# Kernel optimization log

Hardware: AMD Instinct MI355X
Metric: run time of the kernel (lower is better)

## Reference

```python
import jax, jax.numpy as jnp
import numpy as np
from jax import lax


def _gaussian_kernel(sigma=2.0, size=5):
    # matches torch: arange(-size//2 + 1, size//2 + 1) == [-2,-1,0,1,2] for size=5
    r = np.arange(-(size // 2), size // 2 + 1, dtype=np.float32)
    xx, yy = np.meshgrid(r, r, indexing='ij')
    k = np.exp(-(xx ** 2 + yy ** 2) / (2.0 * sigma ** 2))
    return jnp.asarray(k / k.sum(), dtype=jnp.float32)


SCHARR_0 = jnp.array([[3, 0, -3], [10, 0, -10], [3, 0, -3]], dtype=jnp.float32)
SCHARR_90 = jnp.array([[3, 10, 3], [0, 0, 0], [-3, -10, -3]], dtype=jnp.float32)
LAPLACIAN = jnp.array([[0, -1, 0], [-1, 4, -1], [0, -1, 0]], dtype=jnp.float32)
GAUSS = _gaussian_kernel(2.0, 5)
SCHARR_W = 1.0
LAP_W = 0.1


def dwconv(x, k, pad):
    # depthwise conv: x [B,C,H,W], k [kh,kw] shared across channels
    C = x.shape[1]
    kern = jnp.broadcast_to(k[None, None], (C, 1) + k.shape)
    return lax.conv_general_dilated(
        x, kern, window_strides=(1, 1), padding=[(pad, pad), (pad, pad)],
        feature_group_count=C, dimension_numbers=('NCHW', 'OIHW', 'NCHW'))


def conv1x1(x, w, b):
    # x [B,C,H,W], w [O,C], b [O]
    return jnp.einsum('bchw,oc->bohw', x, w) + b[None, :, None, None]


def setup_inputs() -> dict:
    key = jax.random.key(0)
    ks = jax.random.split(key, 6)
    B, C, H, W = 4, 256, 256, 256
    s = 0.05
    return {
        'x': jax.random.normal(ks[0], (B, C, H, W), jnp.float32),
        'w_in': jax.random.normal(ks[1], (64, 256), jnp.float32) * s,
        'b_in': jnp.zeros((64,), jnp.float32),
        'w_fc1': jax.random.normal(ks[2], (4, 64), jnp.float32) * s,
        'b_fc1': jnp.zeros((4,), jnp.float32),
        'w_fc2': jax.random.normal(ks[3], (64, 4), jnp.float32) * s,
        'b_fc2': jnp.zeros((64,), jnp.float32),
        'w_out': jax.random.normal(ks[4], (64, 64), jnp.float32) * s,
        'b_out': jnp.zeros((64,), jnp.float32),
    }


def reference(x, w_in, b_in, w_fc1, b_fc1, w_fc2, b_fc2, w_out, b_out):
    x = conv1x1(x, w_in, b_in)                       # [B,64,H,W]
    sm = dwconv(x, GAUSS, pad=2)                     # gaussian blur
    g0 = dwconv(sm, SCHARR_0, pad=1)
    g90 = dwconv(sm, SCHARR_90, pad=1)
    scharr_mag = SCHARR_W * jnp.maximum(jnp.abs(g0), jnp.abs(g90))
    lap = LAP_W * jnp.abs(dwconv(sm, LAPLACIAN, pad=1))
    edge = scharr_mag + lap
    edge = jnp.clip(edge / (edge.max() + 1e-8), 0.0, 1.0)
    # channel attention (SE)
    pooled = edge.mean(axis=(2, 3), keepdims=True)   # [B,64,1,1]
    h = jax.nn.relu(conv1x1(pooled, w_fc1, b_fc1))
    scale = jax.nn.sigmoid(conv1x1(h, w_fc2, b_fc2))
    edge = edge * scale
    return conv1x1(edge, w_out, b_out)
```

## Files before the change

kernel.cpp:

```cpp
#include <hip/hip_runtime.h>
#include <math.h>


#define HW 65536

#define WS_WT    0ull
#define WS_Y     65536ull
#define WS_EDGE  (65536ull + 67108864ull)
#define WS_SMALL (65536ull + 134217728ull)

__global__ __launch_bounds__(256) void k0_prep(const float* __restrict__ w_in,
                                               float* __restrict__ wT,
                                               unsigned* __restrict__ small) {
    const int tid = threadIdx.x;
    for (int i = tid; i < 512; i += 256) small[i] = 0u;
    for (int i = tid; i < 64 * 256; i += 256) {
        int o = i >> 8, c = i & 255;
        wT[c * 64 + o] = w_in[i];
    }
}

#define K1_COMP(xv, wrp)                                                      \
    {                                                                         \
        float4 w0 = *(const float4*)(wrp);                                    \
        float4 w1 = *(const float4*)((wrp) + 4);                              \
        float4 w2 = *(const float4*)((wrp) + 8);                              \
        float4 w3 = *(const float4*)((wrp) + 12);                             \
        float wf[16] = {w0.x,w0.y,w0.z,w0.w, w1.x,w1.y,w1.z,w1.w,             \
                        w2.x,w2.y,w2.z,w2.w, w3.x,w3.y,w3.z,w3.w};            \
        _Pragma("unroll")                                                     \
        for (int oi = 0; oi < 16; ++oi) {                                     \
            acc[0][oi] = fmaf((xv).x, wf[oi], acc[0][oi]);                    \
            acc[1][oi] = fmaf((xv).y, wf[oi], acc[1][oi]);                    \
            acc[2][oi] = fmaf((xv).z, wf[oi], acc[2][oi]);                    \
            acc[3][oi] = fmaf((xv).w, wf[oi], acc[3][oi]);                    \
        }                                                                     \
    }

__global__ __launch_bounds__(256) void k1_convin(const float* __restrict__ x,
                                                 const float* __restrict__ wT,
                                                 const float* __restrict__ b_in,
                                                 float* __restrict__ y) {
    __shared__ float ws[64 * 64];
    const int tid  = threadIdx.x;
    const int lane = tid & 63;
    const int wv   = tid >> 6;
    const int blk  = blockIdx.x;
    const int b    = blk >> 8;
    const int pbase = ((blk & 255) << 8) + (wv << 6) + ((lane & 15) << 2);
    const int og    = (lane >> 4) << 4;

    const float* xp = x + (size_t)(b << 8) * HW + pbase;

    float acc[4][16];
#pragma unroll
    for (int oi = 0; oi < 16; ++oi) {
        float bv = b_in[og + oi];
        acc[0][oi] = bv; acc[1][oi] = bv; acc[2][oi] = bv; acc[3][oi] = bv;
    }

    float4 xb0 = *(const float4*)(xp + 0 * (size_t)HW);
    float4 xb1 = *(const float4*)(xp + 1 * (size_t)HW);
    float4 xb2 = *(const float4*)(xp + 2 * (size_t)HW);
    float4 xb3 = *(const float4*)(xp + 3 * (size_t)HW);

#pragma unroll 1
    for (int ch = 0; ch < 4; ++ch) {
        __syncthreads();
        const float4* src = (const float4*)(wT + (ch << 6) * 64);
        float4* dst = (float4*)ws;
        for (int i = tid; i < 1024; i += 256) dst[i] = src[i];
        __syncthreads();

#pragma unroll 1
        for (int cc = 0; cc < 64; cc += 4) {
            const int gn = ((ch << 6) + cc + 4) & 255;
            float4 n0 = *(const float4*)(xp + (size_t)(gn    ) * HW);
            float4 n1 = *(const float4*)(xp + (size_t)(gn + 1) * HW);
            float4 n2 = *(const float4*)(xp + (size_t)(gn + 2) * HW);
            float4 n3 = *(const float4*)(xp + (size_t)(gn + 3) * HW);

            const float* wr = ws + (cc << 6) + og;
            K1_COMP(xb0, wr);
            K1_COMP(xb1, wr + 64);
            K1_COMP(xb2, wr + 128);
            K1_COMP(xb3, wr + 192);

            xb0 = n0; xb1 = n1; xb2 = n2; xb3 = n3;
        }
    }

    float* yb = y + (size_t)(b << 6) * HW + pbase;
#pragma unroll
    for (int oi = 0; oi < 16; ++oi) {
        float4 o4 = {acc[0][oi], acc[1][oi], acc[2][oi], acc[3][oi]};
        *(float4*)(yb + (size_t)(og + oi) * HW) = o4;
    }
}

__global__ __launch_bounds__(256) void k2_edge(const float* __restrict__ y,
                                               float* __restrict__ edge,
                                               unsigned* __restrict__ umax,
                                               float* __restrict__ sums) {
    const int lane = threadIdx.x & 63;
    const int task = blockIdx.x * 4 + (threadIdx.x >> 6);
    const int plane = task >> 4;
    const int r0 = (task & 15) << 4;
    const float* yp = y + (size_t)plane * HW;
    float* ep = edge + (size_t)plane * HW;
    const int col4 = lane << 2;

    const float g = 0.60653066f, G = 0.88249690f;
    const float S1 = 2.f * g + 2.f * G + 1.f;
    const float inv2 = 1.f / (S1 * S1);

    float4 h0{}, h1{}, h2{}, h3{}, h4{};
    float4 s0{}, s1{}, s2{};
    float lmax = 0.f, lsum = 0.f;

    for (int j = r0 - 3; j <= r0 + 18; ++j) {
        float4 v = {0.f, 0.f, 0.f, 0.f};
        if (j >= 0 && j < 256) v = *(const float4*)(yp + j * 256 + col4);
        float lz = __shfl(v.z, lane - 1), lw = __shfl(v.w, lane - 1);
        float rx = __shfl(v.x, lane + 1), ry = __shfl(v.y, lane + 1);
        if (lane == 0)  { lz = 0.f; lw = 0.f; }
        if (lane == 63) { rx = 0.f; ry = 0.f; }
        float4 hv;
        hv.x = fmaf(g, lz,  fmaf(G, lw,  fmaf(G, v.y, fmaf(g, v.z, v.x))));
        hv.y = fmaf(g, lw,  fmaf(G, v.x, fmaf(G, v.z, fmaf(g, v.w, v.y))));
        hv.z = fmaf(g, v.x, fmaf(G, v.y, fmaf(G, v.w, fmaf(g, rx, v.z))));
        hv.w = fmaf(g, v.y, fmaf(G, v.z, fmaf(G, rx,  fmaf(g, ry, v.w))));
        h0 = h1; h1 = h2; h2 = h3; h3 = h4; h4 = hv;

        if (j >= r0 + 1) {
            float4 sv;
            sv.x = (g * (h0.x + h4.x) + G * (h1.x + h3.x) + h2.x) * inv2;
            sv.y = (g * (h0.y + h4.y) + G * (h1.y + h3.y) + h2.y) * inv2;
            sv.z = (g * (h0.z + h4.z) + G * (h1.z + h3.z) + h2.z) * inv2;
            sv.w = (g * (h0.w + h4.w) + G * (h1.w + h3.w) + h2.w) * inv2;
            s0 = s1; s1 = s2; s2 = sv;

            if (j >= r0 + 3) {
                const int er = j - 3;
                float4 A = s0, B = s1, C = s2;
                float Alw = __shfl(A.w, lane - 1), Arx = __shfl(A.x, lane + 1);
                float Blw = __shfl(B.w, lane - 1), Brx = __shfl(B.x, lane + 1);
                float Clw = __shfl(C.w, lane - 1), Crx = __shfl(C.x, lane + 1);
                if (lane == 0)  { Alw = 0.f; Blw = 0.f; Clw = 0.f; }
                if (lane == 63) { Arx = 0.f; Brx = 0.f; Crx = 0.f; }
                if (er == 0)   { A = float4{}; Alw = 0.f; Arx = 0.f; }
                if (er == 255) { C = float4{}; Clw = 0.f; Crx = 0.f; }
                float A6[6] = {Alw, A.x, A.y, A.z, A.w, Arx};
                float B6[6] = {Blw, B.x, B.y, B.z, B.w, Brx};
                float C6[6] = {Clw, C.x, C.y, C.z, C.w, Crx};
                float4 e4;
                float* ev = (float*)&e4;
#pragma unroll
                for (int k = 0; k < 4; ++k) {
                    float g0  = 3.f * (A6[k] - A6[k+2]) + 10.f * (B6[k] - B6[k+2])
                              + 3.f * (C6[k] - C6[k+2]);
                    float g90 = 3.f * (A6[k] - C6[k]) + 10.f * (A6[k+1] - C6[k+1])
                              + 3.f * (A6[k+2] - C6[k+2]);
                    float lap = 4.f * B6[k+1] - B6[k] - B6[k+2] - A6[k+1] - C6[k+1];
                    float e = fmaxf(fabsf(g0), fabsf(g90)) + 0.1f * fabsf(lap);
                    ev[k] = e;
                    lmax = fmaxf(lmax, e);
                    lsum += e;
                }
                *(float4*)(ep + er * 256 + col4) = e4;
            }
        }
    }

    for (int off = 32; off > 0; off >>= 1) {
        lmax = fmaxf(lmax, __shfl_down(lmax, off));
        lsum += __shfl_down(lsum, off);
    }
    if (lane == 0) {
        atomicMax(umax, __float_as_uint(lmax));
        atomicAdd(&sums[plane], lsum);
    }
}

__global__ __launch_bounds__(256) void k3_se(const unsigned* __restrict__ umax,
                                             const float* __restrict__ sums,
                                             const float* __restrict__ w_fc1,
                                             const float* __restrict__ b_fc1,
                                             const float* __restrict__ w_fc2,
                                             const float* __restrict__ b_fc2,
                                             const float* __restrict__ w_out,
                                             float* __restrict__ w_eff) {
    const int tid = threadIdx.x;
    const int b = tid >> 6, o = tid & 63;
    const float mx = __uint_as_float(*umax);
    const float inv = 1.f / (mx + 1e-8f);
    __shared__ float coef[256];

    float h[4];
#pragma unroll
    for (int j = 0; j < 4; ++j) h[j] = b_fc1[j];
    for (int c = 0; c < 64; ++c) {
        float pooled = sums[b * 64 + c] * inv * (1.f / 65536.f);
#pragma unroll
        for (int j = 0; j < 4; ++j) h[j] = fmaf(pooled, w_fc1[j * 64 + c], h[j]);
    }
#pragma unroll
    for (int j = 0; j < 4; ++j) h[j] = fmaxf(h[j], 0.f);
    float z = b_fc2[o];
#pragma unroll
    for (int j = 0; j < 4; ++j) z = fmaf(h[j], w_fc2[o * 4 + j], z);
    float sc = 1.f / (1.f + expf(-z));
    coef[tid] = sc * inv;
    __syncthreads();
    for (int c = 0; c < 64; ++c)
        w_eff[((b * 64) + c) * 64 + o] = w_out[o * 64 + c] * coef[b * 64 + c];
}

__global__ __launch_bounds__(256) void k4_out(const float* __restrict__ edge,
                                              const float* __restrict__ w_eff,
                                              const float* __restrict__ b_out,
                                              float* __restrict__ out) {
    __shared__ float ws[64 * 64];
    const int tid  = threadIdx.x;
    const int lane = tid & 63;
    const int wv   = tid >> 6;
    const int blk  = blockIdx.x;
    const int b    = blk >> 8;
    const int pbase = ((blk & 255) << 8) + (wv << 6) + ((lane & 15) << 2);
    const int og    = (lane >> 4) << 4;

    {
        const float4* src = (const float4*)(w_eff + b * 4096);
        float4* dst = (float4*)ws;
        for (int i = tid; i < 1024; i += 256) dst[i] = src[i];
    }

    const float* eb = edge + (size_t)(b << 6) * HW + pbase;
    float acc[4][16];
#pragma unroll
    for (int oi = 0; oi < 16; ++oi) {
        float bv = b_out[og + oi];
        acc[0][oi] = bv; acc[1][oi] = bv; acc[2][oi] = bv; acc[3][oi] = bv;
    }

    float4 xb0 = *(const float4*)(eb + 0 * (size_t)HW);
    float4 xb1 = *(const float4*)(eb + 1 * (size_t)HW);
    float4 xb2 = *(const float4*)(eb + 2 * (size_t)HW);
    float4 xb3 = *(const float4*)(eb + 3 * (size_t)HW);

    __syncthreads();

#pragma unroll 1
    for (int cc = 0; cc < 64; cc += 4) {
        const int gn = (cc + 4) & 63;
        float4 n0 = *(const float4*)(eb + (size_t)(gn    ) * HW);
        float4 n1 = *(const float4*)(eb + (size_t)(gn + 1) * HW);
        float4 n2 = *(const float4*)(eb + (size_t)(gn + 2) * HW);
        float4 n3 = *(const float4*)(eb + (size_t)(gn + 3) * HW);

        const float* wr = ws + (cc << 6) + og;
        K1_COMP(xb0, wr);
        K1_COMP(xb1, wr + 64);
        K1_COMP(xb2, wr + 128);
        K1_COMP(xb3, wr + 192);

        xb0 = n0; xb1 = n1; xb2 = n2; xb3 = n3;
    }

    float* ob = out + (size_t)(b << 6) * HW + pbase;
#pragma unroll
    for (int oi = 0; oi < 16; ++oi) {
        float4 o4 = {acc[0][oi], acc[1][oi], acc[2][oi], acc[3][oi]};
        *(float4*)(ob + (size_t)(og + oi) * HW) = o4;
    }
}

extern "C" void kernel_launch(void* const* d_in, const int* in_sizes, int n_in,
                              void* d_out, int out_size, void* d_ws, size_t ws_size,
                              hipStream_t stream) {
    const float* x     = (const float*)d_in[0];
    const float* w_in  = (const float*)d_in[1];
    const float* b_in  = (const float*)d_in[2];
    const float* w_fc1 = (const float*)d_in[3];
    const float* b_fc1 = (const float*)d_in[4];
    const float* w_fc2 = (const float*)d_in[5];
    const float* b_fc2 = (const float*)d_in[6];
    const float* w_out = (const float*)d_in[7];
    const float* b_out = (const float*)d_in[8];

    char* ws = (char*)d_ws;
    float*    wT    = (float*)(ws + WS_WT);
    float*    y     = (float*)(ws + WS_Y);
    float*    edge  = (float*)(ws + WS_EDGE);
    unsigned* umax  = (unsigned*)(ws + WS_SMALL);
    float*    sums  = (float*)(ws + WS_SMALL + 64);
    float*    w_eff = (float*)(ws + WS_SMALL + 2048);
    float*    out   = (float*)d_out;

    hipLaunchKernelGGL(k0_prep,  dim3(1),    dim3(256), 0, stream, w_in, wT, umax);
    hipLaunchKernelGGL(k1_convin,dim3(1024), dim3(256), 0, stream, x, wT, b_in, y);
    hipLaunchKernelGGL(k2_edge,  dim3(1024), dim3(256), 0, stream, y, edge, umax, sums);
    hipLaunchKernelGGL(k3_se,    dim3(1),    dim3(256), 0, stream, umax, sums,
                       w_fc1, b_fc1, w_fc2, b_fc2, w_out, w_eff);
    hipLaunchKernelGGL(k4_out,   dim3(1024), dim3(256), 0, stream, edge, w_eff, b_out, out);
}
```

Baseline: 558.4 us.

## Remap 1x1 conv waves to output groups with scalar weight loads and drop atomics

After: 496.5 us. 11.1% less time.

```diff
diff --git a/kernel.cpp b/kernel.cpp
--- a/kernel.cpp
+++ b/kernel.cpp
@@ -10,22 +10,20 @@
 #define WS_SMALL (65536ull + 134217728ull)
 
 __global__ __launch_bounds__(256) void k0_prep(const float* __restrict__ w_in,
-                                               float* __restrict__ wT,
-                                               unsigned* __restrict__ small) {
+                                               float* __restrict__ wT) {
     const int tid = threadIdx.x;
-    for (int i = tid; i < 512; i += 256) small[i] = 0u;
     for (int i = tid; i < 64 * 256; i += 256) {
         int o = i >> 8, c = i & 255;
         wT[c * 64 + o] = w_in[i];
     }
 }
 
-#define K1_COMP(xv, wrp)                                                      \
+#define CH_COMP(xv, wrow)                                                     \
     {                                                                         \
-        float4 w0 = *(const float4*)(wrp);                                    \
-        float4 w1 = *(const float4*)((wrp) + 4);                              \
-        float4 w2 = *(const float4*)((wrp) + 8);                              \
-        float4 w3 = *(const float4*)((wrp) + 12);                             \
+        float4 w0 = *(const float4*)(wrow);                                   \
+        float4 w1 = *(const float4*)((wrow) + 4);                             \
+        float4 w2 = *(const float4*)((wrow) + 8);                             \
+        float4 w3 = *(const float4*)((wrow) + 12);                            \
         float wf[16] = {w0.x,w0.y,w0.z,w0.w, w1.x,w1.y,w1.z,w1.w,             \
                         w2.x,w2.y,w2.z,w2.w, w3.x,w3.y,w3.z,w3.w};            \
         _Pragma("unroll")                                                     \
@@ -41,16 +39,15 @@
                                                  const float* __restrict__ wT,
                                                  const float* __restrict__ b_in,
                                                  float* __restrict__ y) {
-    __shared__ float ws[64 * 64];
     const int tid  = threadIdx.x;
     const int lane = tid & 63;
-    const int wv   = tid >> 6;
+    const int og   = __builtin_amdgcn_readfirstlane((tid >> 6) << 4);
     const int blk  = blockIdx.x;
     const int b    = blk >> 8;
-    const int pbase = ((blk & 255) << 8) + (wv << 6) + ((lane & 15) << 2);
-    const int og    = (lane >> 4) << 4;
-
-    const float* xp = x + (size_t)(b << 8) * HW + pbase;
+    const int px   = ((blk & 255) << 8) + (lane << 2);
+
+    const float* xp  = x + (size_t)(b << 8) * HW + px;
+    const float* wTg = wT + og;
 
     float acc[4][16];
 #pragma unroll
@@ -59,49 +56,54 @@
         acc[0][oi] = bv; acc[1][oi] = bv; acc[2][oi] = bv; acc[3][oi] = bv;
     }
 
-    float4 xb0 = *(const float4*)(xp + 0 * (size_t)HW);
-    float4 xb1 = *(const float4*)(xp + 1 * (size_t)HW);
-    float4 xb2 = *(const float4*)(xp + 2 * (size_t)HW);
-    float4 xb3 = *(const float4*)(xp + 3 * (size_t)HW);
+    float4 xr0 = *(const float4*)(xp + 0 * (size_t)HW);
+    float4 xr1 = *(const float4*)(xp + 1 * (size_t)HW);
+    float4 xr2 = *(const float4*)(xp + 2 * (size_t)HW);
+    float4 xr3 = *(const float4*)(xp + 3 * (size_t)HW);
+    float4 xr4 = *(const float4*)(xp + 4 * (size_t)HW);
+    float4 xr5 = *(const float4*)(xp + 5 * (size_t)HW);
+    float4 xr6 = *(const float4*)(xp + 6 * (size_t)HW);
+    float4 xr7 = *(const float4*)(xp + 7 * (size_t)HW);
 
 #pragma unroll 1
-    for (int ch = 0; ch < 4; ++ch) {
-        __syncthreads();
-        const float4* src = (const float4*)(wT + (ch << 6) * 64);
-        float4* dst = (float4*)ws;
-        for (int i = tid; i < 1024; i += 256) dst[i] = src[i];
-        __syncthreads();
-
-#pragma unroll 1
-        for (int cc = 0; cc < 64; cc += 4) {
-            const int gn = ((ch << 6) + cc + 4) & 255;
+    for (int cc = 0; cc < 256; cc += 8) {
+        {
+            const int gn = (cc + 8) & 255;
             float4 n0 = *(const float4*)(xp + (size_t)(gn    ) * HW);
             float4 n1 = *(const float4*)(xp + (size_t)(gn + 1) * HW);
             float4 n2 = *(const float4*)(xp + (size_t)(gn + 2) * HW);
             float4 n3 = *(const float4*)(xp + (size_t)(gn + 3) * HW);
-
-            const float* wr = ws + (cc << 6) + og;
-            K1_COMP(xb0, wr);
-            K1_COMP(xb1, wr + 64);
-            K1_COMP(xb2, wr + 128);
-            K1_COMP(xb3, wr + 192);
-
-            xb0 = n0; xb1 = n1; xb2 = n2; xb3 = n3;
-        }
-    }
-
-    float* yb = y + (size_t)(b << 6) * HW + pbase;
-#pragma unroll
-    for (int oi = 0; oi < 16; ++oi) {
-        float4 o4 = {acc[0][oi], acc[1][oi], acc[2][oi], acc[3][oi]};
-        *(float4*)(yb + (size_t)(og + oi) * HW) = o4;
-    }
+            CH_COMP(xr0, wTg + (size_t)(cc    ) * 64);
+            CH_COMP(xr1, wTg + (size_t)(cc + 1) * 64);
+            CH_COMP(xr2, wTg + (size_t)(cc + 2) * 64);
+            CH_COMP(xr3, wTg + (size_t)(cc + 3) * 64);
+            xr0 = n0; xr1 = n1; xr2 = n2; xr3 = n3;
+        }
+        {
+            const int gn = (cc + 12) & 255;
+            float4 n0 = *(const float4*)(xp + (size_t)(gn    ) * HW);
+            float4 n1 = *(const float4*)(xp + (size_t)(gn + 1) * HW);
+            float4 n2 = *(const float4*)(xp + (size_t)(gn + 2) * HW);
+            float4 n3 = *(const float4*)(xp + (size_t)(gn + 3) * HW);
+            CH_COMP(xr4, wTg + (size_t)(cc + 4) * 64);
+            CH_COMP(xr5, wTg + (size_t)(cc + 5) * 64);
+            CH_COMP(xr6, wTg + (size_t)(cc + 6) * 64);
+            CH_COMP(xr7, wTg + (size_t)(cc + 7) * 64);
+            xr4 = n0; xr5 = n1; xr6 = n2; xr7 = n3;
+        }
+    }
+
+    float* yb = y + (size_t)(b << 6) * HW + px;
+#pragma unroll
+    for (int oi = 0; oi < 16; ++oi)
+        *(float4*)(yb + (size_t)(og + oi) * HW) = float4{acc[0][oi], acc[1][oi],
+                                                         acc[2][oi], acc[3][oi]};
 }
 
 __global__ __launch_bounds__(256) void k2_edge(const float* __restrict__ y,
                                                float* __restrict__ edge,
-                                               unsigned* __restrict__ umax,
-                                               float* __restrict__ sums) {
+                                               float* __restrict__ wavemax,
+                                               float* __restrict__ wavesum) {
     const int lane = threadIdx.x & 63;
     const int task = blockIdx.x * 4 + (threadIdx.x >> 6);
     const int plane = task >> 4;
@@ -118,9 +120,15 @@
     float4 s0{}, s1{}, s2{};
     float lmax = 0.f, lsum = 0.f;
 
+    float4 vcur{};
+    if (r0 - 3 >= 0) vcur = *(const float4*)(yp + (r0 - 3) * 256 + col4);
+
     for (int j = r0 - 3; j <= r0 + 18; ++j) {
-        float4 v = {0.f, 0.f, 0.f, 0.f};
-        if (j >= 0 && j < 256) v = *(const float4*)(yp + j * 256 + col4);
+        float4 vnext{};
+        const int jn = j + 1;
+        if (jn <= r0 + 18 && jn >= 0 && jn < 256)
+            vnext = *(const float4*)(yp + jn * 256 + col4);
+        float4 v = vcur;
         float lz = __shfl(v.z, lane - 1), lw = __shfl(v.w, lane - 1);
         float rx = __shfl(v.x, lane + 1), ry = __shfl(v.y, lane + 1);
         if (lane == 0)  { lz = 0.f; lw = 0.f; }
@@ -170,6 +178,7 @@
                 *(float4*)(ep + er * 256 + col4) = e4;
             }
         }
+        vcur = vnext;
     }
 
     for (int off = 32; off > 0; off >>= 1) {
@@ -177,13 +186,13 @@
         lsum += __shfl_down(lsum, off);
     }
     if (lane == 0) {
-        atomicMax(umax, __float_as_uint(lmax));
-        atomicAdd(&sums[plane], lsum);
-    }
-}
-
-__global__ __launch_bounds__(256) void k3_se(const unsigned* __restrict__ umax,
-                                             const float* __restrict__ sums,
+        wavemax[task] = lmax;
+        wavesum[task] = lsum;
+    }
+}
+
+__global__ __launch_bounds__(256) void k3_se(const float* __restrict__ wavemax,
+                                             const float* __restrict__ wavesum,
                                              const float* __restrict__ w_fc1,
                                              const float* __restrict__ b_fc1,
                                              const float* __restrict__ w_fc2,
@@ -192,15 +201,30 @@
                                              float* __restrict__ w_eff) {
     const int tid = threadIdx.x;
     const int b = tid >> 6, o = tid & 63;
-    const float mx = __uint_as_float(*umax);
+    __shared__ float smax[256];
+    __shared__ float ssum[256];
+    __shared__ float coef[256];
+
+    float m = 0.f;
+    for (int i = tid; i < 4096; i += 256) m = fmaxf(m, wavemax[i]);
+    smax[tid] = m;
+    float ps = 0.f;
+#pragma unroll
+    for (int k = 0; k < 16; ++k) ps += wavesum[tid * 16 + k];
+    ssum[tid] = ps;
+    __syncthreads();
+    for (int s = 128; s > 0; s >>= 1) {
+        if (tid < s) smax[tid] = fmaxf(smax[tid], smax[tid + s]);
+        __syncthreads();
+    }
+    const float mx = smax[0];
     const float inv = 1.f / (mx + 1e-8f);
-    __shared__ float coef[256];
 
     float h[4];
 #pragma unroll
     for (int j = 0; j < 4; ++j) h[j] = b_fc1[j];
     for (int c = 0; c < 64; ++c) {
-        float pooled = sums[b * 64 + c] * inv * (1.f / 65536.f);
+        float pooled = ssum[b * 64 + c] * inv * (1.f / 65536.f);
 #pragma unroll
         for (int j = 0; j < 4; ++j) h[j] = fmaf(pooled, w_fc1[j * 64 + c], h[j]);
     }
@@ -220,22 +244,16 @@
                                               const float* __restrict__ w_eff,
                                               const float* __restrict__ b_out,
                                               float* __restrict__ out) {
-    __shared__ float ws[64 * 64];
     const int tid  = threadIdx.x;
     const int lane = tid & 63;
-    const int wv   = tid >> 6;
+    const int og   = __builtin_amdgcn_readfirstlane((tid >> 6) << 4);
     const int blk  = blockIdx.x;
     const int b    = blk >> 8;
-    const int pbase = ((blk & 255) << 8) + (wv << 6) + ((lane & 15) << 2);
-    const int og    = (lane >> 4) << 4;
-
-    {
-        const float4* src = (const float4*)(w_eff + b * 4096);
-        float4* dst = (float4*)ws;
-        for (int i = tid; i < 1024; i += 256) dst[i] = src[i];
-    }
-
-    const float* eb = edge + (size_t)(b << 6) * HW + pbase;
+    const int px   = ((blk & 255) << 8) + (lane << 2);
+
+    const float* eb  = edge + (size_t)(b << 6) * HW + px;
+    const float* wTg = w_eff + (b << 12) + og;
+
     float acc[4][16];
 #pragma unroll
     for (int oi = 0; oi < 16; ++oi) {
@@ -243,36 +261,48 @@
         acc[0][oi] = bv; acc[1][oi] = bv; acc[2][oi] = bv; acc[3][oi] = bv;
     }
 
-    float4 xb0 = *(const float4*)(eb + 0 * (size_t)HW);
-    float4 xb1 = *(const float4*)(eb + 1 * (size_t)HW);
-    float4 xb2 = *(const float4*)(eb + 2 * (size_t)HW);
-    float4 xb3 = *(const float4*)(eb + 3 * (size_t)HW);
-
-    __syncthreads();
+    float4 xr0 = *(const float4*)(eb + 0 * (size_t)HW);
+    float4 xr1 = *(const float4*)(eb + 1 * (size_t)HW);
+    float4 xr2 = *(const float4*)(eb + 2 * (size_t)HW);
+    float4 xr3 = *(const float4*)(eb + 3 * (size_t)HW);
+    float4 xr4 = *(const float4*)(eb + 4 * (size_t)HW);
+    float4 xr5 = *(const float4*)(eb + 5 * (size_t)HW);
+    float4 xr6 = *(const float4*)(eb + 6 * (size_t)HW);
+    float4 xr7 = *(const float4*)(eb + 7 * (size_t)HW);
 
 #pragma unroll 1
-    for (int cc = 0; cc < 64; cc += 4) {
-        const int gn = (cc + 4) & 63;
-        float4 n0 = *(const float4*)(eb + (size_t)(gn    ) * HW);
-        float4 n1 = *(const float4*)(eb + (size_t)(gn + 1) * HW);
-        float4 n2 = *(const float4*)(eb + (size_t)(gn + 2) * HW);
-        float4 n3 = *(const float4*)(eb + (size_t)(gn + 3) * HW);
-
-        const float* wr = ws + (cc << 6) + og;
-        K1_COMP(xb0, wr);
-        K1_COMP(xb1, wr + 64);
-        K1_COMP(xb2, wr + 128);
-        K1_COMP(xb3, wr + 192);
-
-        xb0 = n0; xb1 = n1; xb2 = n2; xb3 = n3;
-    }
-
-    float* ob = out + (size_t)(b << 6) * HW + pbase;
-#pragma unroll
-    for (int oi = 0; oi < 16; ++oi) {
-        float4 o4 = {acc[0][oi], acc[1][oi], acc[2][oi], acc[3][oi]};
-        *(float4*)(ob + (size_t)(og + oi) * HW) = o4;
-    }
+    for (int cc = 0; cc < 64; cc += 8) {
+        {
+            const int gn = (cc + 8) & 63;
+            float4 n0 = *(const float4*)(eb + (size_t)(gn    ) * HW);
+            float4 n1 = *(const float4*)(eb + (size_t)(gn + 1) * HW);
+            float4 n2 = *(const float4*)(eb + (size_t)(gn + 2) * HW);
+            float4 n3 = *(const float4*)(eb + (size_t)(gn + 3) * HW);
+            CH_COMP(xr0, wTg + (size_t)(cc    ) * 64);
+            CH_COMP(xr1, wTg + (size_t)(cc + 1) * 64);
+            CH_COMP(xr2, wTg + (size_t)(cc + 2) * 64);
+            CH_COMP(xr3, wTg + (size_t)(cc + 3) * 64);
+            xr0 = n0; xr1 = n1; xr2 = n2; xr3 = n3;
+        }
+        {
+            const int gn = (cc + 12) & 63;
+            float4 n0 = *(const float4*)(eb + (size_t)(gn    ) * HW);
+            float4 n1 = *(const float4*)(eb + (size_t)(gn + 1) * HW);
+            float4 n2 = *(const float4*)(eb + (size_t)(gn + 2) * HW);
+            float4 n3 = *(const float4*)(eb + (size_t)(gn + 3) * HW);
+            CH_COMP(xr4, wTg + (size_t)(cc + 4) * 64);
+            CH_COMP(xr5, wTg + (size_t)(cc + 5) * 64);
+            CH_COMP(xr6, wTg + (size_t)(cc + 6) * 64);
+            CH_COMP(xr7, wTg + (size_t)(cc + 7) * 64);
+            xr4 = n0; xr5 = n1; xr6 = n2; xr7 = n3;
+        }
+    }
+
+    float* ob = out + (size_t)(b << 6) * HW + px;
+#pragma unroll
+    for (int oi = 0; oi < 16; ++oi)
+        *(float4*)(ob + (size_t)(og + oi) * HW) = float4{acc[0][oi], acc[1][oi],
+                                                         acc[2][oi], acc[3][oi]};
 }
 
 extern "C" void kernel_launch(void* const* d_in, const int* in_sizes, int n_in,
@@ -289,18 +319,18 @@
     const float* b_out = (const float*)d_in[8];
 
     char* ws = (char*)d_ws;
-    float*    wT    = (float*)(ws + WS_WT);
-    float*    y     = (float*)(ws + WS_Y);
-    float*    edge  = (float*)(ws + WS_EDGE);
-    unsigned* umax  = (unsigned*)(ws + WS_SMALL);
-    float*    sums  = (float*)(ws + WS_SMALL + 64);
-    float*    w_eff = (float*)(ws + WS_SMALL + 2048);
-    float*    out   = (float*)d_out;
-
-    hipLaunchKernelGGL(k0_prep,  dim3(1),    dim3(256), 0, stream, w_in, wT, umax);
+    float* wT      = (float*)(ws + WS_WT);
+    float* y       = (float*)(ws + WS_Y);
+    float* edge    = (float*)(ws + WS_EDGE);
+    float* wavemax = (float*)(ws + WS_SMALL);
+    float* wavesum = (float*)(ws + WS_SMALL + 16384);
+    float* w_eff   = (float*)(ws + WS_SMALL + 32768);
+    float* out     = (float*)d_out;
+
+    hipLaunchKernelGGL(k0_prep,  dim3(1),    dim3(256), 0, stream, w_in, wT);
     hipLaunchKernelGGL(k1_convin,dim3(1024), dim3(256), 0, stream, x, wT, b_in, y);
-    hipLaunchKernelGGL(k2_edge,  dim3(1024), dim3(256), 0, stream, y, edge, umax, sums);
-    hipLaunchKernelGGL(k3_se,    dim3(1),    dim3(256), 0, stream, umax, sums,
+    hipLaunchKernelGGL(k2_edge,  dim3(1024), dim3(256), 0, stream, y, edge, wavemax, wavesum);
+    hipLaunchKernelGGL(k3_se,    dim3(1),    dim3(256), 0, stream, wavemax, wavesum,
                        w_fc1, b_fc1, w_fc2, b_fc2, w_out, w_eff);
     hipLaunchKernelGGL(k4_out,   dim3(1024), dim3(256), 0, stream, edge, w_eff, b_out, out);
 }
```
